# Performance work log

Measured on AMD Instinct MI355X. Metric: run time of the kernel, lower is better.

## Reference

```python
import jax, jax.numpy as jnp
import numpy as np

NUM_CAPSULE = 16
DIM_CAPSULE = 16
NUM_ROUTINGS = 3
EPS = 1e-7  # K.epsilon()


def squash(v, axis=-1):
    # vectors * ||v||^2 / ((1+||v||^2) * ||v||)
    sn = jnp.sum(v * v, axis=axis, keepdims=True)
    return v * (sn / ((1.0 + sn) * jnp.sqrt(sn + EPS)))


def setup_inputs() -> dict:
    key = jax.random.key(0)
    k1, k2 = jax.random.split(key)
    B, I, Din = 64, 2048, 8
    inputs = jax.random.normal(k1, (B, I, Din), dtype=jnp.float32)
    # he_normal init: std = sqrt(2 / fan_in), fan_in = Din
    W = jax.random.normal(k2, (I, NUM_CAPSULE, Din, DIM_CAPSULE), dtype=jnp.float32) * np.float32(np.sqrt(2.0 / Din))
    return {"inputs": inputs, "W": W}


def reference(inputs, W):
    # inputs: [B, I, Din]; W: [I, K, Din, Dout]
    # u_hat[b,i,k,:] = inputs[b,i,:] @ W[i,k,:,:]  (replaces tile + per-batch matmul scan)
    u_hat = jnp.einsum('bid,ikde->bike', inputs, W)  # [B, I, K, Dout]
    B, I, Kc, _ = u_hat.shape
    b = jnp.zeros((B, I, Kc), dtype=u_hat.dtype)  # routing logits (bias)
    v = None
    for r in range(NUM_ROUTINGS):
        c = jax.nn.softmax(b, axis=2)                       # coupling over output capsules
        s = jnp.einsum('bik,bike->bke', c, u_hat)           # weighted sum over input capsules
        v = squash(s)                                       # [B, K, Dout]
        if r < NUM_ROUTINGS - 1:
            b = b + jnp.einsum('bike,bke->bik', u_hat, v)   # agreement update
    return v  # [B, num_capsule, dim_capsule]
```

## Files before the change

### kernel.cpp

```cpp
#include <hip/hip_runtime.h>
#include <hip/hip_cooperative_groups.h>
#include <cstddef>

namespace cg = cooperative_groups;

constexpr int Bn = 64;
constexpr int In = 2048;
constexpr int Dk = 8;
constexpr int Kc = 16;
constexpr int En = 16;
constexpr float EPS = 1e-7f;

constexpr int IB   = 8;
constexpr int P    = In / IB;
constexpr int BSET = 16;
constexpr int NBG  = Bn / BSET;
constexpr int BLOCKS = P * NBG;
constexpr int THREADS = 256;
constexpr int PPX  = P / 8;

typedef float v2f __attribute__((ext_vector_type(2)));
__device__ __forceinline__ v2f fma2(v2f a, v2f b, v2f c) {
    return __builtin_elementwise_fma(a, b, c);
}
__device__ __forceinline__ v2f splat2(float s) { return (v2f){s, s}; }

template<int CTRL>
__device__ __forceinline__ float dpp_add(float v) {
    int r = __builtin_amdgcn_update_dpp(0, __float_as_int(v), CTRL, 0xF, 0xF, true);
    return v + __int_as_float(r);
}

template<bool UNIFORM>
__device__ __forceinline__ void iter_body(const float* __restrict__ smemx,
        const float* __restrict__ W, const float* __restrict__ vsg,
        float* __restrict__ partial, int p, int b0, int i0, int t)
{
    const int lane = t & 63;
    const int wvi  = t >> 6;
    const int k    = lane >> 2;
    const int e4   = (lane & 3) << 2;
    const int bw   = b0 + (wvi << 2);

    v2f vlo[4], vhi[4];
    if (!UNIFORM) {
        #pragma unroll
        for (int b4 = 0; b4 < 4; ++b4) {
            const float4 vv = *(const float4*)(vsg + ((bw + b4) << 8) + k * 16 + e4);
            vlo[b4] = (v2f){vv.x, vv.y};
            vhi[b4] = (v2f){vv.z, vv.w};
        }
    }

    v2f alo[4], ahi[4];
    #pragma unroll
    for (int b4 = 0; b4 < 4; ++b4) { alo[b4] = (v2f){0.f, 0.f}; ahi[b4] = (v2f){0.f, 0.f}; }

    #pragma unroll 2
    for (int ii = 0; ii < IB; ++ii) {
        const int i = i0 + ii;
        const float* wp = W + (size_t)i * (Kc * Dk * En) + k * (Dk * En) + e4;
        v2f wlo[8], whi[8];
        #pragma unroll
        for (int d = 0; d < 8; ++d) {
            const float4 wv = *(const float4*)(wp + d * En);
            wlo[d] = (v2f){wv.x, wv.y};
            whi[d] = (v2f){wv.z, wv.w};
        }

        #pragma unroll
        for (int b4 = 0; b4 < 4; ++b4) {
            const int bl = (wvi << 2) + b4;
            const float* xp = smemx + (((bl << 3) + ii) << 3);
            const float4 x0 = *(const float4*)xp;
            const float4 x1 = *(const float4*)(xp + 4);
            const float xs8[8] = {x0.x, x0.y, x0.z, x0.w, x1.x, x1.y, x1.z, x1.w};

            v2f ulo = (v2f){0.f, 0.f}, uhi = (v2f){0.f, 0.f};
            #pragma unroll
            for (int d = 0; d < 8; ++d) {
                const v2f xd = splat2(xs8[d]);
                ulo = fma2(xd, wlo[d], ulo);
                uhi = fma2(xd, whi[d], uhi);
            }

            if (UNIFORM) {
                alo[b4] += ulo;
                ahi[b4] += uhi;
            } else {
                v2f t2 = ulo * vlo[b4];
                t2 = fma2(uhi, vhi[b4], t2);
                float tt = t2.x + t2.y;
                tt = dpp_add<0xB1>(tt);
                tt = dpp_add<0x4E>(tt);
                const float pe = __expf(tt);
                float den = dpp_add<0x124>(pe);
                den = dpp_add<0x128>(den);
                den += __shfl_xor(den, 16);
                den += __shfl_xor(den, 32);
                const float c = pe * __builtin_amdgcn_rcpf(den);
                const v2f cc = splat2(c);
                alo[b4] = fma2(cc, ulo, alo[b4]);
                ahi[b4] = fma2(cc, uhi, ahi[b4]);
            }
        }
    }

    #pragma unroll
    for (int b4 = 0; b4 < 4; ++b4) {
        *(float4*)(partial + ((size_t)(bw + b4) * P + p) * 256 + k * 16 + e4) =
            make_float4(alo[b4].x, alo[b4].y, ahi[b4].x, ahi[b4].y);
    }
}

__device__ __forceinline__ void reduce_phase(float* red,
        const float* __restrict__ partial, float scale,
        const float* __restrict__ vprev, float* __restrict__ vout, int rb, int t)
{
    const int b  = rb >> 2;
    const int q  = rb & 3;
    const int t4 = t & 63;
    const int pg = t >> 6;
    const int el = (q << 6) + t4;
    const float* pp = partial + (size_t)b * (P * 256) + ((pg << 6) * 256) + el;

    float s0 = 0.f, s1 = 0.f, s2 = 0.f, s3 = 0.f;
    #pragma unroll 4
    for (int j = 0; j < 64; j += 4) {
        s0 += pp[(j + 0) * 256];
        s1 += pp[(j + 1) * 256];
        s2 += pp[(j + 2) * 256];
        s3 += pp[(j + 3) * 256];
    }
    red[(pg << 6) + t4] = (s0 + s1) + (s2 + s3);
    __syncthreads();

    if (t < 64) {
        const float val = (red[t4] + red[64 + t4] + red[128 + t4] + red[192 + t4]) * scale;
        float sq = val * val;
        sq += __shfl_xor(sq, 1);
        sq += __shfl_xor(sq, 2);
        sq += __shfl_xor(sq, 4);
        sq += __shfl_xor(sq, 8);
        const float f = sq / ((1.0f + sq) * sqrtf(sq + EPS));
        float v = val * f;
        if (vprev) v += vprev[(b << 8) + el];
        vout[(b << 8) + el] = v;
    }
    __syncthreads();
}

__device__ __forceinline__ void tile_map(int bid, int& p, int& b0, int& i0) {
    const int xcd = bid & 7;
    const int j   = bid >> 3;
    p  = xcd * PPX + (j & (PPX - 1));
    b0 = (j >> 5) * BSET;
    i0 = p * IB;
}

__device__ __forceinline__ void stage_x(float* smem, const float* __restrict__ x,
                                        int b0, int i0, int t) {
    const int bl = t >> 4;
    const int r  = t & 15;
    ((float4*)smem)[t] = *(const float4*)(x + ((size_t)(b0 + bl) * In + i0) * Dk + (r << 2));
}

__global__ __launch_bounds__(THREADS)
void caps_fused(const float* __restrict__ x, const float* __restrict__ W,
                float* __restrict__ partial, float* __restrict__ v0,
                float* __restrict__ vs, float* __restrict__ out)
{
    cg::grid_group grid = cg::this_grid();
    __shared__ __align__(16) float smem[1280];

    const int t = threadIdx.x, bid = blockIdx.x;
    int p, b0, i0;
    tile_map(bid, p, b0, i0);

    stage_x(smem, x, b0, i0, t);
    __syncthreads();

    iter_body<true>(smem, W, nullptr, partial, p, b0, i0, t);
    grid.sync();
    if (bid < 256) reduce_phase(smem + 1024, partial, 1.0f / 16.0f, nullptr, v0, bid, t);
    grid.sync();

    iter_body<false>(smem, W, v0, partial, p, b0, i0, t);
    grid.sync();
    if (bid < 256) reduce_phase(smem + 1024, partial, 1.0f, v0, vs, bid, t);
    grid.sync();

    iter_body<false>(smem, W, vs, partial, p, b0, i0, t);
    grid.sync();
    if (bid < 256) reduce_phase(smem + 1024, partial, 1.0f, nullptr, out, bid, t);
}

template<bool UNIFORM>
__global__ __launch_bounds__(THREADS)
void caps_iter_g(const float* __restrict__ x, const float* __restrict__ W,
                 const float* __restrict__ vsg, float* __restrict__ partial)
{
    __shared__ __align__(16) float smem[1024];
    const int t = threadIdx.x;
    int p, b0, i0;
    tile_map(blockIdx.x, p, b0, i0);
    stage_x(smem, x, b0, i0, t);
    __syncthreads();
    iter_body<UNIFORM>(smem, W, vsg, partial, p, b0, i0, t);
}

__global__ __launch_bounds__(THREADS)
void caps_reduce_g(const float* __restrict__ partial, float scale,
                   const float* __restrict__ vprev, float* __restrict__ vout)
{
    __shared__ __align__(16) float red[256];
    reduce_phase(red, partial, scale, vprev, vout, blockIdx.x, threadIdx.x);
}

extern "C" void kernel_launch(void* const* d_in, const int* in_sizes, int n_in,
                              void* d_out, int out_size, void* d_ws, size_t ws_size,
                              hipStream_t stream) {
    const float* x = (const float*)d_in[0];
    const float* W = (const float*)d_in[1];
    float* out = (float*)d_out;
    float* ws  = (float*)d_ws;

    float* v0      = ws;
    float* vs      = ws + 16384;
    float* partial = ws + 32768;

    int dev = 0;
    hipGetDevice(&dev);
    int numCU = 0;
    hipDeviceGetAttribute(&numCU, hipDeviceAttributeMultiprocessorCount, dev);
    int maxB = 0;
    hipError_t oe = hipOccupancyMaxActiveBlocksPerMultiprocessor(
        &maxB, (const void*)caps_fused, THREADS, 0);
    const bool coop = (oe == hipSuccess) && numCU > 0 &&
                      ((long)maxB * numCU >= BLOCKS);

    if (coop) {
        void* args[] = { (void*)&x, (void*)&W, (void*)&partial,
                         (void*)&v0, (void*)&vs, (void*)&out };
        hipLaunchCooperativeKernel((void*)caps_fused, dim3(BLOCKS), dim3(THREADS),
                                   args, 0, stream);
    } else {
        caps_iter_g<true ><<<BLOCKS, THREADS, 0, stream>>>(x, W, nullptr, partial);
        caps_reduce_g<<<256, THREADS, 0, stream>>>(partial, 1.0f / 16.0f, nullptr, v0);
        caps_iter_g<false><<<BLOCKS, THREADS, 0, stream>>>(x, W, v0, partial);
        caps_reduce_g<<<256, THREADS, 0, stream>>>(partial, 1.0f, v0, vs);
        caps_iter_g<false><<<BLOCKS, THREADS, 0, stream>>>(x, W, vs, partial);
        caps_reduce_g<<<256, THREADS, 0, stream>>>(partial, 1.0f, nullptr, out);
    }
}
```

Baseline: 64.25 us.

## Replace cooperative grid.sync with hierarchical per-XCD atomic grid barrier

Swaps the cooperative-groups grid.sync calls for a custom two-level barrier. Blocks first increment a per-XCD counter, and the last arriver on each XCD bumps a global counter that every block polls with s_sleep. After a reduce phase only the 256 reducing blocks arrive, so the other blocks just wait. This is meant to cut grid-sync overhead and atomic contention, at the cost of a memset launch per call to clear the counters and reliance on every block being co-resident.

```diff
diff --git a/kernel.cpp b/kernel.cpp
--- a/kernel.cpp
+++ b/kernel.cpp
@@ -1,8 +1,6 @@
 #include <hip/hip_runtime.h>
 #include <hip/hip_cooperative_groups.h>
 #include <cstddef>
-
-namespace cg = cooperative_groups;
 
 constexpr int Bn = 64;
 constexpr int In = 2048;
@@ -29,6 +27,30 @@
 __device__ __forceinline__ float dpp_add(float v) {
     int r = __builtin_amdgcn_update_dpp(0, __float_as_int(v), CTRL, 0xF, 0xF, true);
     return v + __int_as_float(r);
+}
+
+__device__ __forceinline__ void grid_bar(int* __restrict__ bar, int phase,
+                                         int bid, int t, bool arrive,
+                                         int per_xcd_target)
+{
+    __syncthreads();
+    if (t == 0) {
+        int* slot = bar + phase * 256;
+        if (arrive) {
+            __threadfence();
+            const int xcd = bid & 7;
+            const int prev = __hip_atomic_fetch_add(slot + xcd * 16, 1,
+                    __ATOMIC_ACQ_REL, __HIP_MEMORY_SCOPE_AGENT);
+            if (prev == per_xcd_target - 1)
+                __hip_atomic_fetch_add(slot + 240, 1,
+                        __ATOMIC_ACQ_REL, __HIP_MEMORY_SCOPE_AGENT);
+        }
+        while (__hip_atomic_load(slot + 240, __ATOMIC_ACQUIRE,
+                                 __HIP_MEMORY_SCOPE_AGENT) < 8)
+            __builtin_amdgcn_s_sleep(2);
+        __threadfence();
+    }
+    __syncthreads();
 }
 
 template<bool UNIFORM>
@@ -167,10 +189,10 @@
 
 __global__ __launch_bounds__(THREADS)
 void caps_fused(const float* __restrict__ x, const float* __restrict__ W,
-                float* __restrict__ partial, float* __restrict__ v0,
-                float* __restrict__ vs, float* __restrict__ out)
-{
-    cg::grid_group grid = cg::this_grid();
+                int* __restrict__ bar, float* __restrict__ partial,
+                float* __restrict__ v0, float* __restrict__ vs,
+                float* __restrict__ out)
+{
     __shared__ __align__(16) float smem[1280];
 
     const int t = threadIdx.x, bid = blockIdx.x;
@@ -181,17 +203,17 @@
     __syncthreads();
 
     iter_body<true>(smem, W, nullptr, partial, p, b0, i0, t);
-    grid.sync();
+    grid_bar(bar, 0, bid, t, true, 128);
     if (bid < 256) reduce_phase(smem + 1024, partial, 1.0f / 16.0f, nullptr, v0, bid, t);
-    grid.sync();
+    grid_bar(bar, 1, bid, t, bid < 256, 32);
 
     iter_body<false>(smem, W, v0, partial, p, b0, i0, t);
-    grid.sync();
+    grid_bar(bar, 2, bid, t, true, 128);
     if (bid < 256) reduce_phase(smem + 1024, partial, 1.0f, v0, vs, bid, t);
-    grid.sync();
+    grid_bar(bar, 3, bid, t, bid < 256, 32);
 
     iter_body<false>(smem, W, vs, partial, p, b0, i0, t);
-    grid.sync();
+    grid_bar(bar, 4, bid, t, true, 128);
     if (bid < 256) reduce_phase(smem + 1024, partial, 1.0f, nullptr, out, bid, t);
 }
 
@@ -225,9 +247,10 @@
     float* out = (float*)d_out;
     float* ws  = (float*)d_ws;
 
-    float* v0      = ws;
-    float* vs      = ws + 16384;
-    float* partial = ws + 32768;
+    int*   bar     = (int*)ws;
+    float* v0      = ws + 2048;
+    float* vs      = ws + 2048 + 16384;
+    float* partial = ws + 2048 + 32768;
 
     int dev = 0;
     hipGetDevice(&dev);
@@ -240,7 +263,8 @@
                       ((long)maxB * numCU >= BLOCKS);
 
     if (coop) {
-        void* args[] = { (void*)&x, (void*)&W, (void*)&partial,
+        hipMemsetAsync(bar, 0, 2048 * sizeof(int), stream);
+        void* args[] = { (void*)&x, (void*)&W, (void*)&bar, (void*)&partial,
                          (void*)&v0, (void*)&vs, (void*)&out };
         hipLaunchCooperativeKernel((void*)caps_fused, dim3(BLOCKS), dim3(THREADS),
                                    args, 0, stream);
```

Result: no change. 64.67 us (+0.7%).
